# Performance work log

Hardware: AMD Instinct MI355X
Metric: run time of the kernel (lower is better)

The kernel has to match this reference:

```python
import jax, jax.numpy as jnp
import numpy as np

# Fixed hyperparameters from init_kwargs
KH, KW = 3, 3
GRID_SIZE = 5
SPLINE_ORDER = 3
GRID_RANGE = (-1.0, 1.0)


def _make_grid():
    # grid buffer: arange(-k, grid_size + k + 1) * h + grid_range[0], shape (G + 2k + 1,) = (12,)
    h = (GRID_RANGE[1] - GRID_RANGE[0]) / GRID_SIZE
    return (jnp.arange(-SPLINE_ORDER, GRID_SIZE + SPLINE_ORDER + 1, dtype=jnp.float32) * h
            + GRID_RANGE[0])


def _unfold(x):
    # torch.nn.Unfold with kernel (3,3), stride 1, pad 0, dilation 1.
    # Returns (N, C*KH*KW) with channel-major ordering (c, i, j), matching torch.
    B, C, H, W = x.shape
    Ho, Wo = H - KH + 1, W - KW + 1
    cols = [x[:, :, i:i + Ho, j:j + Wo] for i in range(KH) for j in range(KW)]
    p = jnp.stack(cols, axis=2)                    # (B, C, KH*KW, Ho, Wo)
    p = p.reshape(B, C * KH * KW, Ho * Wo)         # (B, in_features, L)
    p = p.transpose(0, 2, 1).reshape(-1, C * KH * KW)  # (B*L, in_features)
    return p, Ho, Wo


def _b_splines(x, grid):
    # x: (N, in_features); grid: (G + 2k + 1,) uniform, shared across features.
    # Returns (N, in_features, G + k) B-spline basis via Cox-de Boor recursion.
    x = x[..., None]  # (N, in, 1)
    bases = ((x >= grid[:-1]) & (x < grid[1:])).astype(x.dtype)  # (N, in, G+2k)
    for k in range(1, SPLINE_ORDER + 1):
        left = (x - grid[: -(k + 1)]) / (grid[k:-1] - grid[: -(k + 1)])
        right = (grid[k + 1:] - x) / (grid[k + 1:] - grid[1:-k])
        bases = left * bases[..., :-1] + right * bases[..., 1:]
    return bases  # (N, in, G + k)


def setup_inputs() -> dict:
    key = jax.random.key(0)
    k1, k2, k3, k4 = jax.random.split(key, 4)
    in_features = 32 * KH * KW  # 288
    out_features = 64
    n_coef = GRID_SIZE + SPLINE_ORDER  # 8
    x = jax.random.normal(k1, (16, 32, 64, 64), dtype=jnp.float32)
    base_weight = jax.random.normal(k2, (out_features, in_features), dtype=jnp.float32) * (1.0 / np.sqrt(in_features))
    spline_weight = jax.random.normal(k3, (out_features, in_features, n_coef), dtype=jnp.float32) * 0.1
    spline_scaler = jax.random.normal(k4, (out_features, in_features), dtype=jnp.float32) * (1.0 / np.sqrt(in_features))
    return {"x": x, "base_weight": base_weight, "spline_weight": spline_weight,
            "spline_scaler": spline_scaler}


def reference(x, base_weight, spline_weight, spline_scaler):
    B = x.shape[0]
    out_features = base_weight.shape[0]
    grid = _make_grid()

    patches, Ho, Wo = _unfold(x)                              # (N, in_features)
    N, in_features = patches.shape

    # KANLinear forward
    base_out = jnp.matmul(jax.nn.relu(patches), base_weight.T)  # (N, out)
    bases = _b_splines(patches, grid)                           # (N, in, G+k)
    scaled_w = spline_weight * spline_scaler[..., None]         # (out, in, G+k)
    spline_out = jnp.matmul(bases.reshape(N, -1), scaled_w.reshape(out_features, -1).T)
    out = base_out + spline_out                                 # (N, out)

    out = out.reshape(B, Ho, Wo, out_features).transpose(0, 3, 1, 2)  # (B, C_out, Ho, Wo)
    return out
```

## Files before the change

kernel.cpp:

```cpp
#include <hip/hip_runtime.h>
#include <stdint.h>

typedef _Float16 half8  __attribute__((ext_vector_type(8)));
typedef float    f32x4  __attribute__((ext_vector_type(4)));
typedef uint32_t u32x4  __attribute__((ext_vector_type(4)));

#define FIN  288
#define NOUT 64
#define LPB  3844
#define KSPL 72
#define NBF  20736
#define NBAS (16*64*32*64)
#define NXR  (16*64*64*4)
#define PADS 16

#define SCL  200
#define LDSL (31*SCL + 2*64 + 64 + 8)


__device__ inline half8 bspline8(float xv) {
  float u = fmaf(xv, 2.5f, 5.5f);
  float fi = floorf(u);
  int i = (int)fi;
  float t = u - fi, s = 1.0f - t;
  float t2 = t * t, t3 = t2 * t;
  float s2 = s * s, s3 = s2 * s;
  float w3 = t3 * 0.16666667f;
  float w0 = s3 * 0.16666667f;
  float w1 = fmaf(0.5f, t3, -t2) + 0.66666667f;
  float w2 = fmaf(0.5f, s3, -s2) + 0.66666667f;
  uint32_t u01 = __builtin_bit_cast(uint32_t, __builtin_amdgcn_cvt_pkrtz(w0, w1));
  uint32_t u23 = __builtin_bit_cast(uint32_t, __builtin_amdgcn_cvt_pkrtz(w2, w3));
  uint64_t V = (uint64_t)u01 | ((uint64_t)u23 << 32);
  uint32_t vl = (uint32_t)(V << 16);
  u32x4 fr;
#pragma unroll
  for (int q = 0; q < 4; ++q) {
    int d = i - 2 * q;
    uint32_t rr = (uint32_t)(V >> ((48 - 16 * d) & 63));
    fr[q] = ((uint32_t)d <= 3u) ? rr : ((d == 4) ? vl : 0u);
  }
  return __builtin_bit_cast(half8, fr);
}

__global__ __launch_bounds__(256) void prep_all(const float* __restrict__ x,
                                                const float* __restrict__ bw,
                                                const float* __restrict__ sw,
                                                const float* __restrict__ sc,
                                                half8* __restrict__ ws) {
  int bid = blockIdx.x;
  if (bid < 2048) {
    int t = bid * 256 + threadIdx.x;
    int w4 = t & 15;
    int cperm = (t >> 4) & 31;
    int bh = t >> 9;
    int c = ((cperm & 7) << 2) | (cperm >> 3);
    const float4 v = *(const float4*)(x + (bh >> 6) * 131072 + c * 4096 +
                                      (bh & 63) * 64 + w4 * 4);
    half8* dst = ws + NBF + (size_t)t * 4;
    dst[0] = bspline8(v.x);
    dst[1] = bspline8(v.y);
    dst[2] = bspline8(v.z);
    dst[3] = bspline8(v.w);
  } else if (bid < 3072) {
    int t = (bid - 2048) * 256 + threadIdx.x;
    int quad = t & 3;
    int w = (t >> 2) & 63;
    int bh = t >> 8;
    const float* xp = x + (bh >> 6) * 131072 + (quad * 8) * 4096 + (bh & 63) * 64 + w;
    half8 v;
#pragma unroll
    for (int j = 0; j < 8; ++j) v[j] = (_Float16)fmaxf(xp[j * 4096], 0.0f);
    ws[NBF + NBAS + t] = v;
  } else {
    int t = (bid - 3072) * 256 + threadIdx.x;
    half8 v;
    int dst;
    if (t < NOUT * FIN) {
      int o = t / FIN;
      int f = t - o * FIN;
      float scale = sc[t];
      const float* p = sw + t * 8;
#pragma unroll
      for (int c = 0; c < 8; ++c) v[c] = (_Float16)(p[c] * scale);
      int ch = f / 9;
      int r  = f - ch * 9;
      int ii = r / 3;
      int jj = r - ii * 3;
      int g  = ch >> 2, q = ch & 3;
      int kt = ii * 24 + jj * 8 + g;
      dst = (kt * 4 + (o >> 4)) * 64 + q * 16 + (o & 15);
    } else {
      int t2 = t - NOUT * FIN;
      int lane = t2 & 63;
      int nf = (t2 >> 6) & 3;
      int ktb = t2 >> 8;
      int o = nf * 16 + (lane & 15);
      int q = lane >> 4;
      int i2 = ktb / 3;
      int j2 = ktb - 3 * i2;
#pragma unroll
      for (int c0 = 0; c0 < 8; ++c0)
        v[c0] = (_Float16)bw[o * FIN + 9 * (q * 8 + c0) + 3 * i2 + j2];
      dst = ((KSPL + ktb) * 4 + nf) * 64 + lane;
    }
    ws[dst] = v;
  }
}

__global__ __launch_bounds__(256, 2) void kan_main(
    const half8* __restrict__ ws,
    float* __restrict__ out) {
  const half8* __restrict__ bfrag = ws;
  const half8* __restrict__ bas   = ws + NBF;
  const half8* __restrict__ xr    = ws + NBF + NBAS;

  const int tid = threadIdx.x;
  int bid0 = blockIdx.x;
  int bid = (bid0 & 7) * 32 + (bid0 >> 3);
  const int b  = bid >> 4;
  const int hg = bid & 15;
  const int nfb = blockIdx.y * 2;

  const int lane = tid & 63;
  const int wv   = tid >> 6;
  const int quad = lane >> 4;
  const int m16  = lane & 15;
  const int ho   = hg * 4 + wv;
  const int hoc  = ho < 61 ? ho : 61;

  f32x4 acc[4][2];
#pragma unroll
  for (int mt = 0; mt < 4; ++mt)
#pragma unroll
    for (int nf = 0; nf < 2; ++nf) acc[mt][nf] = (f32x4){0.f, 0.f, 0.f, 0.f};

  const half8* bb = bas + ((b * 64 + hoc) * 32 + quad * 8) * 64 + m16;
  for (int ii = 0; ii < 3; ++ii) {
    for (int jj = 0; jj < 3; ++jj) {
      const half8* p   = bb + ii * 2048 + jj;
      const half8* bfp = bfrag + (ii * 24 + jj * 8) * 256 + nfb * 64 + lane;
#pragma unroll
      for (int g = 0; g < 8; ++g) {
        half8 af[4];
#pragma unroll
        for (int mt = 0; mt < 4; ++mt) af[mt] = p[g * 64 + mt * 16];
#pragma unroll
        for (int nf = 0; nf < 2; ++nf) {
          half8 bf = bfp[g * 256 + nf * 64];
#pragma unroll
          for (int mt = 0; mt < 4; ++mt)
            acc[mt][nf] = __builtin_amdgcn_mfma_f32_16x16x32_f16(af[mt], bf, acc[mt][nf], 0, 0, 0);
        }
      }
    }
  }

  for (int kb = 0; kb < 9; ++kb) {
    int i2 = (kb * 11) >> 5;
    int j2 = kb - 3 * i2;
    const half8* q = xr + ((b * 64 + hoc + i2) * 64 + m16 + j2) * 4 + quad;
    half8 af[4];
#pragma unroll
    for (int mt = 0; mt < 4; ++mt) af[mt] = q[mt * 64];
    const half8* bfp = bfrag + (KSPL + kb) * 256 + nfb * 64 + lane;
#pragma unroll
    for (int nf = 0; nf < 2; ++nf) {
      half8 bf = bfp[nf * 64];
#pragma unroll
      for (int mt = 0; mt < 4; ++mt)
        acc[mt][nf] = __builtin_amdgcn_mfma_f32_16x16x32_f16(af[mt], bf, acc[mt][nf], 0, 0, 0);
    }
  }

  if (ho < 62) {
    float* ob = out + b * (NOUT * LPB) + ho * 62;
#pragma unroll
    for (int mt = 0; mt < 4; ++mt) {
#pragma unroll
      for (int rg = 0; rg < 4; ++rg) {
        int wo2 = mt * 16 + quad * 4 + rg;
        if (wo2 < 62) {
#pragma unroll
          for (int nf = 0; nf < 2; ++nf) {
            int o = (nfb + nf) * 16 + m16;
            ob[o * LPB + wo2] = acc[mt][nf][rg];
          }
        }
      }
    }
  }
}

__global__ void prep_bfrag_legacy(const float* __restrict__ bw,
                                  const float* __restrict__ sw,
                                  const float* __restrict__ sc,
                                  half8* __restrict__ bfrag) {
  int t = blockIdx.x * 256 + threadIdx.x;
  half8 v;
  int dst;
  if (t < NOUT * FIN) {
    int o = t / FIN;
    int f = t - o * FIN;
    float scale = sc[t];
    const float* p = sw + t * 8;
#pragma unroll
    for (int c = 0; c < 8; ++c) v[c] = (_Float16)(p[c] * scale);
    int ch = f / 9;
    int r  = f - ch * 9;
    int ii = r / 3;
    int jj = r - ii * 3;
    int g  = ch >> 2, q = ch & 3;
    int kt = ii * 24 + jj * 8 + g;
    dst = (kt * 4 + (o >> 4)) * 64 + q * 16 + (o & 15);
  } else {
    int t2 = t - NOUT * FIN;
    int lane = t2 & 63;
    int nf = (t2 >> 6) & 3;
    int ktb = t2 >> 8;
    int o = nf * 16 + (lane & 15);
    int f0 = ktb * 32 + (lane >> 4) * 8;
    const float* p = bw + o * FIN + f0;
#pragma unroll
    for (int c = 0; c < 8; ++c) v[c] = (_Float16)p[c];
    dst = ((KSPL + ktb) * 4 + nf) * 64 + lane;
  }
  bfrag[dst] = v;
}

__global__ __launch_bounds__(256, 4) void kan_main_legacy(
    const float* __restrict__ x,
    const half8* __restrict__ bfrag,
    float* __restrict__ out) {
  __shared__ float lx[LDSL];
  const int tid = threadIdx.x;
  const int bid = blockIdx.x;
  const int b  = bid / 62;
  const int ho = bid - b * 62;
  const float* xb = x + b * 131072 + ho * 64;
#pragma unroll
  for (int r = 0; r < 6; ++r) {
    int gid = r * 256 + tid;
    int row = gid >> 4;
    int c   = (row * 683) >> 11;
    int ii  = row - c * 3;
    int colv = (gid & 15) * 4;
    const float4 v = *(const float4*)(xb + c * 4096 + ii * 64 + colv);
    *(float4*)(&lx[c * SCL + ii * 64 + colv]) = v;
  }
  __syncthreads();
  const int lane = tid & 63;
  const int wv   = tid >> 6;
  const int quad = lane >> 4;
  const int m16  = lane & 15;
  const int wo   = wv * 16 + m16;
  f32x4 acc[4];
#pragma unroll
  for (int nf = 0; nf < 4; ++nf) acc[nf] = (f32x4){0.f, 0.f, 0.f, 0.f};
  int kt = 0;
#pragma unroll
  for (int ii = 0; ii < 3; ++ii) {
#pragma unroll
    for (int jj = 0; jj < 3; ++jj) {
      const float* lbase = lx + quad * SCL + ii * 64 + wo + jj;
#pragma unroll
      for (int g = 0; g < 8; ++g) {
        float xv = lbase[g * (4 * SCL)];
        half8 af = bspline8(xv);
#pragma unroll
        for (int nf = 0; nf < 4; ++nf) {
          half8 bf = bfrag[(kt * 4 + nf) * 64 + lane];
          acc[nf] = __builtin_amdgcn_mfma_f32_16x16x32_f16(af, bf, acc[nf], 0, 0, 0);
        }
        ++kt;
      }
    }
  }
#pragma unroll
  for (int kb = 0; kb < 9; ++kb) {
    int f0 = kb * 32 + quad * 8;
    half8 a;
#pragma unroll
    for (int j = 0; j < 8; ++j) {
      int f = f0 + j;
      int c = (f * 57) >> 9;
      int r = f - c * 9;
      int i2 = (r * 11) >> 5;
      int j2 = r - i2 * 3;
      a[j] = (_Float16)fmaxf(lx[c * SCL + i2 * 64 + wo + j2], 0.0f);
    }
#pragma unroll
    for (int nf = 0; nf < 4; ++nf) {
      half8 bf = bfrag[((KSPL + kb) * 4 + nf) * 64 + lane];
      acc[nf] = __builtin_amdgcn_mfma_f32_16x16x32_f16(a, bf, acc[nf], 0, 0, 0);
    }
  }
  float* ob = out + b * (NOUT * LPB) + ho * 62;
#pragma unroll
  for (int rg = 0; rg < 4; ++rg) {
    int wo2 = wv * 16 + quad * 4 + rg;
    if (wo2 < 62) {
#pragma unroll
      for (int nf = 0; nf < 4; ++nf) {
        int o = nf * 16 + m16;
        ob[o * LPB + wo2] = acc[nf][rg];
      }
    }
  }
}

extern "C" void kernel_launch(void* const* d_in, const int* in_sizes, int n_in,
                              void* d_out, int out_size, void* d_ws, size_t ws_size,
                              hipStream_t stream) {
  const float* x  = (const float*)d_in[0];
  const float* bw = (const float*)d_in[1];
  const float* sw = (const float*)d_in[2];
  const float* sc = (const float*)d_in[3];
  float* out = (float*)d_out;
  half8* ws = (half8*)d_ws;

  const size_t need = (size_t)(NBF + NBAS + NXR + PADS) * sizeof(half8);
  if (ws_size >= need) {
    prep_all<<<3153, 256, 0, stream>>>(x, bw, sw, sc, ws);
    kan_main<<<dim3(256, 2), 256, 0, stream>>>(ws, out);
  } else {
    prep_bfrag_legacy<<<81, 256, 0, stream>>>(bw, sw, sc, ws);
    kan_main_legacy<<<16 * 62, 256, 0, stream>>>(x, ws, out);
  }
}
```

Baseline: 132.1 us.

## Split K dimension across two wave groups with LDS reduction in kan_main

Doubles the block to 512 threads and splits the spline K loop across two groups of four waves. The second group also handles the base-weight term, then writes its partial accumulators to shared memory. After a barrier the first group adds them and stores the output. The aim is more waves in flight to hide global load latency on this latency-bound kernel, at the cost of about 36KB of LDS per block, a barrier, and an uneven split of work between the two groups.

```diff
diff --git a/kernel.cpp b/kernel.cpp
--- a/kernel.cpp
+++ b/kernel.cpp
@@ -108,9 +108,11 @@
   }
 }
 
-__global__ __launch_bounds__(256, 2) void kan_main(
+#define REDSTR 36
+__global__ __launch_bounds__(512, 4) void kan_main(
     const half8* __restrict__ ws,
     float* __restrict__ out) {
+  __shared__ float red[4 * 64 * REDSTR];
   const half8* __restrict__ bfrag = ws;
   const half8* __restrict__ bas   = ws + NBF;
   const half8* __restrict__ xr    = ws + NBF + NBAS;
@@ -124,9 +126,11 @@
 
   const int lane = tid & 63;
   const int wv   = tid >> 6;
+  const int g2   = wv >> 2;
+  const int rw   = wv & 3;
   const int quad = lane >> 4;
   const int m16  = lane & 15;
-  const int ho   = hg * 4 + wv;
+  const int ho   = hg * 4 + rw;
   const int hoc  = ho < 61 ? ho : 61;
 
   f32x4 acc[4][2];
@@ -136,55 +140,76 @@
     for (int nf = 0; nf < 2; ++nf) acc[mt][nf] = (f32x4){0.f, 0.f, 0.f, 0.f};
 
   const half8* bb = bas + ((b * 64 + hoc) * 32 + quad * 8) * 64 + m16;
-  for (int ii = 0; ii < 3; ++ii) {
-    for (int jj = 0; jj < 3; ++jj) {
-      const half8* p   = bb + ii * 2048 + jj;
-      const half8* bfp = bfrag + (ii * 24 + jj * 8) * 256 + nfb * 64 + lane;
-#pragma unroll
-      for (int g = 0; g < 8; ++g) {
-        half8 af[4];
-#pragma unroll
-        for (int mt = 0; mt < 4; ++mt) af[mt] = p[g * 64 + mt * 16];
-#pragma unroll
-        for (int nf = 0; nf < 2; ++nf) {
-          half8 bf = bfp[g * 256 + nf * 64];
-#pragma unroll
-          for (int mt = 0; mt < 4; ++mt)
-            acc[mt][nf] = __builtin_amdgcn_mfma_f32_16x16x32_f16(af[mt], bf, acc[mt][nf], 0, 0, 0);
-        }
-      }
-    }
-  }
-
-  for (int kb = 0; kb < 9; ++kb) {
-    int i2 = (kb * 11) >> 5;
-    int j2 = kb - 3 * i2;
-    const half8* q = xr + ((b * 64 + hoc + i2) * 64 + m16 + j2) * 4 + quad;
-    half8 af[4];
-#pragma unroll
-    for (int mt = 0; mt < 4; ++mt) af[mt] = q[mt * 64];
-    const half8* bfp = bfrag + (KSPL + kb) * 256 + nfb * 64 + lane;
-#pragma unroll
-    for (int nf = 0; nf < 2; ++nf) {
-      half8 bf = bfp[nf * 64];
-#pragma unroll
-      for (int mt = 0; mt < 4; ++mt)
-        acc[mt][nf] = __builtin_amdgcn_mfma_f32_16x16x32_f16(af[mt], bf, acc[mt][nf], 0, 0, 0);
-    }
-  }
-
-  if (ho < 62) {
-    float* ob = out + b * (NOUT * LPB) + ho * 62;
-#pragma unroll
-    for (int mt = 0; mt < 4; ++mt) {
-#pragma unroll
-      for (int rg = 0; rg < 4; ++rg) {
-        int wo2 = mt * 16 + quad * 4 + rg;
-        if (wo2 < 62) {
-#pragma unroll
-          for (int nf = 0; nf < 2; ++nf) {
-            int o = (nfb + nf) * 16 + m16;
-            ob[o * LPB + wo2] = acc[mt][nf][rg];
+  const int plo = g2 ? 5 : 0;
+  const int phi = g2 ? 9 : 5;
+  for (int pp = plo; pp < phi; ++pp) {
+    int ii = (pp * 11) >> 5;
+    int jj = pp - 3 * ii;
+    const half8* p   = bb + ii * 2048 + jj;
+    const half8* bfp = bfrag + (pp * 8) * 256 + nfb * 64 + lane;
+#pragma unroll
+    for (int g = 0; g < 8; ++g) {
+      half8 af[4];
+#pragma unroll
+      for (int mt = 0; mt < 4; ++mt) af[mt] = p[g * 64 + mt * 16];
+#pragma unroll
+      for (int nf = 0; nf < 2; ++nf) {
+        half8 bf = bfp[g * 256 + nf * 64];
+#pragma unroll
+        for (int mt = 0; mt < 4; ++mt)
+          acc[mt][nf] = __builtin_amdgcn_mfma_f32_16x16x32_f16(af[mt], bf, acc[mt][nf], 0, 0, 0);
+      }
+    }
+  }
+
+  if (g2) {
+    for (int kb = 0; kb < 9; ++kb) {
+      int i2 = (kb * 11) >> 5;
+      int j2 = kb - 3 * i2;
+      const half8* q = xr + ((b * 64 + hoc + i2) * 64 + m16 + j2) * 4 + quad;
+      half8 af[4];
+#pragma unroll
+      for (int mt = 0; mt < 4; ++mt) af[mt] = q[mt * 64];
+      const half8* bfp = bfrag + (KSPL + kb) * 256 + nfb * 64 + lane;
+#pragma unroll
+      for (int nf = 0; nf < 2; ++nf) {
+        half8 bf = bfp[nf * 64];
+#pragma unroll
+        for (int mt = 0; mt < 4; ++mt)
+          acc[mt][nf] = __builtin_amdgcn_mfma_f32_16x16x32_f16(af[mt], bf, acc[mt][nf], 0, 0, 0);
+      }
+    }
+    int base = (rw * 64 + lane) * REDSTR;
+#pragma unroll
+    for (int mt = 0; mt < 4; ++mt)
+#pragma unroll
+      for (int nf = 0; nf < 2; ++nf)
+        *(f32x4*)&red[base + (mt * 2 + nf) * 4] = acc[mt][nf];
+  }
+
+  __syncthreads();
+
+  if (!g2) {
+    int base = (rw * 64 + lane) * REDSTR;
+#pragma unroll
+    for (int mt = 0; mt < 4; ++mt)
+#pragma unroll
+      for (int nf = 0; nf < 2; ++nf)
+        acc[mt][nf] += *(const f32x4*)&red[base + (mt * 2 + nf) * 4];
+
+    if (ho < 62) {
+      float* ob = out + b * (NOUT * LPB) + ho * 62;
+#pragma unroll
+      for (int mt = 0; mt < 4; ++mt) {
+#pragma unroll
+        for (int rg = 0; rg < 4; ++rg) {
+          int wo2 = mt * 16 + quad * 4 + rg;
+          if (wo2 < 62) {
+#pragma unroll
+            for (int nf = 0; nf < 2; ++nf) {
+              int o = (nfb + nf) * 16 + m16;
+              ob[o * LPB + wo2] = acc[mt][nf][rg];
+            }
           }
         }
       }
@@ -322,7 +347,7 @@
   const size_t need = (size_t)(NBF + NBAS + NXR + PADS) * sizeof(half8);
   if (ws_size >= need) {
     prep_all<<<3153, 256, 0, stream>>>(x, bw, sw, sc, ws);
-    kan_main<<<dim3(256, 2), 256, 0, stream>>>(ws, out);
+    kan_main<<<dim3(256, 2), 512, 0, stream>>>(ws, out);
   } else {
     prep_bfrag_legacy<<<81, 256, 0, stream>>>(bw, sw, sc, ws);
     kan_main_legacy<<<16 * 62, 256, 0, stream>>>(x, ws, out);
```

Result: no change. 130.2 us (-1.5%).
